# Optimization experiments

Hardware: AMD Instinct MI355X
Metric: run time of the kernel (lower is better)

## Reference

```python
import jax, jax.numpy as jnp
import numpy as np
from jax import lax

B, T, C = 4, 2048, 2048
H, S = 32, 64
HEAD_SIZE_DIVISOR = 8.0
LN_EPS = 1e-5


def setup_inputs() -> dict:
    key = jax.random.key(0)
    ks = jax.random.split(key, 12)
    scale = 0.02
    return {
        "hidden": jax.random.normal(ks[0], (B, T, C), jnp.float32),
        "state_kv": jnp.zeros((B, H, S, S), jnp.float32),
        "time_decay": jax.random.normal(ks[1], (H, S), jnp.float32) * 0.5,
        "time_faaaa": jax.random.normal(ks[2], (H, S), jnp.float32) * 0.5,
        "time_mix_key": jax.random.uniform(ks[3], (1, 1, C), jnp.float32),
        "time_mix_value": jax.random.uniform(ks[4], (1, 1, C), jnp.float32),
        "time_mix_receptance": jax.random.uniform(ks[5], (1, 1, C), jnp.float32),
        "time_mix_gate": jax.random.uniform(ks[6], (1, 1, C), jnp.float32),
        "key_w": jax.random.normal(ks[7], (C, C), jnp.float32) * scale,
        "value_w": jax.random.normal(ks[8], (C, C), jnp.float32) * scale,
        "receptance_w": jax.random.normal(ks[9], (C, C), jnp.float32) * scale,
        "gate_w": jax.random.normal(ks[10], (C, C), jnp.float32) * scale,
        "output_w": jax.random.normal(ks[11], (C, C), jnp.float32) * scale,
        "ln_w": jnp.ones((C,), jnp.float32),
        "ln_b": jnp.zeros((C,), jnp.float32),
    }


def _rwkv5_scan(r, k, v, w, u, state0):
    # r,k,v: [B,T,H,S]; w,u: [H,S]; state0: [B,H,S,S]
    w_ = w[None, :, :, None]  # decay broadcast over value dim
    u_ = u[None, :, :, None]  # time_first (bonus) broadcast over value dim

    def step(state, rkv):
        rt, kt, vt = rkv  # each [B,H,S]
        a = kt[:, :, :, None] * vt[:, :, None, :]      # outer product [B,H,S,S]
        o = jnp.einsum("bhs,bhsd->bhd", rt, u_ * a + state)
        state = a + w_ * state
        return state, o

    rt = jnp.moveaxis(r, 1, 0)  # [T,B,H,S]
    kt = jnp.moveaxis(k, 1, 0)
    vt = jnp.moveaxis(v, 1, 0)
    state_f, out = lax.scan(step, state0, (rt, kt, vt))
    return jnp.moveaxis(out, 0, 1), state_f  # [B,T,H,S], [B,H,S,S]


def reference(hidden, state_kv, time_decay, time_faaaa, time_mix_key,
              time_mix_value, time_mix_receptance, time_mix_gate,
              key_w, value_w, receptance_w, gate_w, output_w, ln_w, ln_b):
    B_, T_, C_ = hidden.shape
    H_, S_ = time_faaaa.shape

    # time shift: prepend zero row, drop last (state=None path)
    shifted = jnp.pad(hidden, ((0, 0), (1, 0), (0, 0)))[:, :-1]

    mix = lambda m: hidden * m + shifted * (1.0 - m)
    k = mix(time_mix_key) @ key_w.T
    v = mix(time_mix_value) @ value_w.T
    r = mix(time_mix_receptance) @ receptance_w.T
    gate = jax.nn.silu(mix(time_mix_gate) @ gate_w.T)

    r = r.reshape(B_, T_, H_, S_)
    k = k.reshape(B_, T_, H_, S_)
    v = v.reshape(B_, T_, H_, S_)

    w = jnp.exp(-jnp.exp(time_decay))  # [H,S]
    out, state_f = _rwkv5_scan(r, k, v, w, time_faaaa, state_kv)

    # GroupNorm over H groups of size S, applied per (b,t) row
    x = out.reshape(B_ * T_, H_, S_) / HEAD_SIZE_DIVISOR
    mu = jnp.mean(x, axis=-1, keepdims=True)
    var = jnp.var(x, axis=-1, keepdims=True)
    xn = (x - mu) * lax.rsqrt(var + LN_EPS)
    xn = xn.reshape(B_ * T_, H_ * S_) * ln_w + ln_b

    out = xn.reshape(B_, T_, C_) * gate
    out = out @ output_w.T
    return out, state_f
```

## Files before the change

kernel.cpp:

```cpp
#include <hip/hip_runtime.h>
#include <hip/hip_bf16.h>

typedef unsigned short u16;
typedef __bf16 bf16x8 __attribute__((ext_vector_type(8)));
typedef unsigned short ushort8v __attribute__((ext_vector_type(8)));
typedef float f32x4 __attribute__((ext_vector_type(4)));
typedef float f32x8 __attribute__((ext_vector_type(8)));

#define B_ 4
#define T_ 2048
#define C_ 2048
#define H_ 32
#define S_ 64

__device__ __forceinline__ u16 f2bf(float x) {
  unsigned int u = __float_as_uint(x);
  unsigned int r = (u + 0x7fffu + ((u >> 16) & 1u)) >> 16;
  return (u16)r;
}
__device__ __forceinline__ float bf2f(u16 x) {
  return __uint_as_float(((unsigned int)x) << 16);
}
__device__ __forceinline__ void gload_lds16(const void* g, void* l) {
  __builtin_amdgcn_global_load_lds(
      (const __attribute__((address_space(1))) void*)g,
      (__attribute__((address_space(3))) void*)l, 16, 0, 0);
}

#define VM10 asm volatile("s_waitcnt vmcnt(10)" ::: "memory")
#define VM8 asm volatile("s_waitcnt vmcnt(8)" ::: "memory")
#define VM4 asm volatile("s_waitcnt vmcnt(4)" ::: "memory")
#define VM0 asm volatile("s_waitcnt vmcnt(0)" ::: "memory")
#define BARR __builtin_amdgcn_s_barrier()
#define SCB __builtin_amdgcn_sched_barrier(0)

__global__ __launch_bounds__(256) void mix_cast_kernel(
    const float* __restrict__ hidden, const float* __restrict__ mixp,
    u16* __restrict__ out) {
  int idx = blockIdx.x * 256 + threadIdx.x;
  int c4 = idx & 511;
  int bt = idx >> 9;
  int t = bt & (T_ - 1);
  float4 h = reinterpret_cast<const float4*>(hidden)[idx];
  float4 m = reinterpret_cast<const float4*>(mixp)[c4];
  float4 sh = make_float4(0.f, 0.f, 0.f, 0.f);
  if (t != 0) sh = reinterpret_cast<const float4*>(hidden)[idx - 512];
  ushort4 o;
  o.x = f2bf(h.x * m.x + sh.x * (1.f - m.x));
  o.y = f2bf(h.y * m.y + sh.y * (1.f - m.y));
  o.z = f2bf(h.z * m.z + sh.z * (1.f - m.z));
  o.w = f2bf(h.w * m.w + sh.w * (1.f - m.w));
  reinterpret_cast<ushort4*>(out)[idx] = o;
}

__global__ __launch_bounds__(256) void mix4_cast_kernel(
    const float* __restrict__ hidden,
    const float* __restrict__ mK, const float* __restrict__ mV,
    const float* __restrict__ mR, const float* __restrict__ mG,
    u16* __restrict__ oK, u16* __restrict__ oV,
    u16* __restrict__ oR, u16* __restrict__ oG) {
  int idx = blockIdx.x * 256 + threadIdx.x;
  int c4 = idx & 511;
  int bt = idx >> 9;
  int t = bt & (T_ - 1);
  float4 h = reinterpret_cast<const float4*>(hidden)[idx];
  float4 sh = make_float4(0.f, 0.f, 0.f, 0.f);
  if (t != 0) sh = reinterpret_cast<const float4*>(hidden)[idx - 512];
  float4 m;
  ushort4 o;
#define DOMIX(MP, OP)                                          \
  m = reinterpret_cast<const float4*>(MP)[c4];                 \
  o.x = f2bf(h.x * m.x + sh.x * (1.f - m.x));                  \
  o.y = f2bf(h.y * m.y + sh.y * (1.f - m.y));                  \
  o.z = f2bf(h.z * m.z + sh.z * (1.f - m.z));                  \
  o.w = f2bf(h.w * m.w + sh.w * (1.f - m.w));                  \
  reinterpret_cast<ushort4*>(OP)[idx] = o;
  DOMIX(mK, oK)
  DOMIX(mV, oV)
  DOMIX(mR, oR)
  DOMIX(mG, oG)
#undef DOMIX
}

__global__ __launch_bounds__(256) void conv_bf16_kernel(
    const float* __restrict__ in, u16* __restrict__ out, int n4) {
  int i = blockIdx.x * 256 + threadIdx.x;
  if (i >= n4) return;
  float4 v = reinterpret_cast<const float4*>(in)[i];
  ushort4 o;
  o.x = f2bf(v.x); o.y = f2bf(v.y); o.z = f2bf(v.z); o.w = f2bf(v.w);
  reinterpret_cast<ushort4*>(out)[i] = o;
}

template <typename OT>
__global__ __launch_bounds__(512, 2) void gemm_bt256(
    const u16* __restrict__ A, const u16* __restrict__ Bm,
    OT* __restrict__ C, int M, int N, int K) {
  __shared__ u16 Asl[4][8192];
  __shared__ u16 Bsl[4][8192];
  const int tid = threadIdx.x, lane = tid & 63, w = tid >> 6;
  const int wr = w >> 2, wc = w & 3;
  const int nbn = N >> 8;
  const int nwg = gridDim.x, bid = blockIdx.x, cpx = nwg >> 3;
  const int swz = (bid & 7) * cpx + (bid >> 3);
  const int bm = swz / nbn, bn = swz % nbn;
  const int Ar0 = bm * 256, Br0 = bn * 256;

  const int rowoff = w * 32 + (lane >> 2);
  const int colswz = ((lane & 3) ^ ((lane >> 3) & 3)) * 8;
  const u16* Agl = A + (size_t)(Ar0 + rowoff) * K + colswz;
  const u16* Bgl = Bm + (size_t)(Br0 + rowoff) * K + colswz;
  const int lb = w * 1024;

  const int rdc = (((lane >> 4) ^ ((lane >> 1) & 3))) * 8;
  const int arow = wr * 128 + (lane & 15);
  const int brow = wc * 64 + (lane & 15);

  f32x4 acc[8][4];
#pragma unroll
  for (int m = 0; m < 8; m++)
#pragma unroll
    for (int n = 0; n < 4; n++) acc[m][n] = (f32x4){0.f, 0.f, 0.f, 0.f};

  auto STA = [&](int ktile, int kk, int slot) {
    const u16* g = Agl + ktile * 64 + kk * 32;
    gload_lds16(g, &Asl[slot][lb]);
    gload_lds16(g + (size_t)16 * K, &Asl[slot][lb + 512]);
  };
  auto STB = [&](int ktile, int kk, int slot) {
    const u16* g = Bgl + ktile * 64 + kk * 32;
    gload_lds16(g, &Bsl[slot][lb]);
    gload_lds16(g + (size_t)16 * K, &Bsl[slot][lb + 512]);
  };
  auto PH = [&](int P, int kk, int mh) {
    const u16* As_ = Asl[P * 2 + kk];
    const u16* Bs_ = Bsl[P * 2 + kk];
    bf16x8 af[4], bv[4];
    int ab = (arow + mh * 64) * 32 + rdc;
#pragma unroll
    for (int mf = 0; mf < 4; mf++)
      af[mf] = __builtin_bit_cast(bf16x8, *reinterpret_cast<const ushort8v*>(&As_[ab + mf * 512]));
    int bb = brow * 32 + rdc;
#pragma unroll
    for (int nf = 0; nf < 4; nf++)
      bv[nf] = __builtin_bit_cast(bf16x8, *reinterpret_cast<const ushort8v*>(&Bs_[bb + nf * 512]));
    __builtin_amdgcn_s_setprio(1);
#pragma unroll
    for (int mf = 0; mf < 4; mf++)
#pragma unroll
      for (int nf = 0; nf < 4; nf++)
        acc[mh * 4 + mf][nf] =
            __builtin_amdgcn_mfma_f32_16x16x32_bf16(af[mf], bv[nf], acc[mh * 4 + mf][nf], 0, 0, 0);
    __builtin_amdgcn_s_setprio(0);
  };

  const int NT = K >> 6;
  STA(0, 0, 0); STB(0, 0, 0);
  STA(0, 1, 1); STB(0, 1, 1);
  STA(1, 0, 2); STB(1, 0, 2);

  for (int T = 0; T + 2 < NT; ++T) {
    int P = T & 1, Q = P ^ 1;
    STA(T + 1, 1, Q * 2 + 1); VM10; BARR; SCB; PH(P, 0, 0); BARR;
    STB(T + 1, 1, Q * 2 + 1); VM10; BARR; SCB; PH(P, 0, 1); BARR;
    STA(T + 2, 0, P * 2 + 0); VM10; BARR; SCB; PH(P, 1, 0); BARR;
    STB(T + 2, 0, P * 2 + 0); VM10; BARR; SCB; PH(P, 1, 1); BARR;
  }
  {
    int T = NT - 2, P = T & 1, Q = P ^ 1;
    STA(T + 1, 1, Q * 2 + 1); VM10; BARR; SCB; PH(P, 0, 0); BARR;
    STB(T + 1, 1, Q * 2 + 1); VM10; BARR; SCB; PH(P, 0, 1); BARR;
    VM8; BARR; SCB; PH(P, 1, 0); BARR;
    VM8; BARR; SCB; PH(P, 1, 1); BARR;
  }
  {
    int P = (NT - 1) & 1;
    VM4; BARR; SCB; PH(P, 0, 0); BARR;
    VM4; BARR; SCB; PH(P, 0, 1); BARR;
    VM0; BARR; SCB; PH(P, 1, 0); BARR;
    VM0; BARR; SCB; PH(P, 1, 1);
  }

  int crow0 = Ar0 + wr * 128 + (lane >> 4) * 4;
  int ccol0 = Br0 + wc * 64 + (lane & 15);
#pragma unroll
  for (int mfg = 0; mfg < 8; mfg++) {
#pragma unroll
    for (int q = 0; q < 4; q++) {
      OT* cp = C + (size_t)(crow0 + mfg * 16 + q) * N + ccol0;
#pragma unroll
      for (int nf = 0; nf < 4; nf++) {
        if constexpr (sizeof(OT) == 2)
          cp[nf * 16] = (OT)f2bf(acc[mfg][nf][q]);
        else
          cp[nf * 16] = (OT)acc[mfg][nf][q];
      }
    }
  }
}

template <int CHL>
__global__ __launch_bounds__(128) void scan_phase1_mfma(
    const u16* __restrict__ Kb, const u16* __restrict__ Vb,
    const float* __restrict__ td, float* __restrict__ chunks) {
  constexpr int NCH = T_ / CHL;
  constexpr int LDW = CHL + 8;
  __shared__ u16 Ash[2][64 * LDW];
  __shared__ u16 Vsh[2][64 * LDW];
  int lane = threadIdx.x & 63, wib = threadIdx.x >> 6;
  int gw = blockIdx.x * 2 + wib;
  int c = gw & (NCH - 1), bh = gw / NCH;
  int h = bh & 31, b = bh >> 5;

  size_t base = ((size_t)b * T_ + (size_t)c * CHL) * C_ + h * 64 + lane;
  const u16* Kp = Kb + base;
  const u16* Vp = Vb + base;

  {
    float w = __expf(-__expf(td[h * 64 + lane]));
    u16* Arow = &Ash[wib][lane * LDW];
    float p = 1.f;
#pragma unroll
    for (int i4 = CHL - 4; i4 >= 0; i4 -= 4) {
      float a3 = bf2f(Kp[(size_t)(i4 + 3) * C_]) * p; p *= w;
      float a2 = bf2f(Kp[(size_t)(i4 + 2) * C_]) * p; p *= w;
      float a1 = bf2f(Kp[(size_t)(i4 + 1) * C_]) * p; p *= w;
      float a0 = bf2f(Kp[(size_t)(i4 + 0) * C_]) * p; p *= w;
      ushort4 pk;
      pk.x = f2bf(a0); pk.y = f2bf(a1); pk.z = f2bf(a2); pk.w = f2bf(a3);
      *reinterpret_cast<ushort4*>(&Arow[i4]) = pk;
    }
  }
  {
    u16* Vrow = &Vsh[wib][lane * LDW];
#pragma unroll
    for (int i4 = 0; i4 < CHL; i4 += 4) {
      ushort4 pk;
      pk.x = Vp[(size_t)(i4 + 0) * C_];
      pk.y = Vp[(size_t)(i4 + 1) * C_];
      pk.z = Vp[(size_t)(i4 + 2) * C_];
      pk.w = Vp[(size_t)(i4 + 3) * C_];
      *reinterpret_cast<ushort4*>(&Vrow[i4]) = pk;
    }
  }

  f32x4 acc[4][4];
#pragma unroll
  for (int m = 0; m < 4; m++)
#pragma unroll
    for (int n = 0; n < 4; n++) acc[m][n] = (f32x4){0.f, 0.f, 0.f, 0.f};

#pragma unroll
  for (int kb = 0; kb < CHL / 32; kb++) {
    int ko = kb * 32 + (lane >> 4) * 8;
    bf16x8 Af[4], Bf[4];
#pragma unroll
    for (int m = 0; m < 4; m++) {
      ushort8v t8 = *reinterpret_cast<const ushort8v*>(&Ash[wib][(m * 16 + (lane & 15)) * LDW + ko]);
      Af[m] = __builtin_bit_cast(bf16x8, t8);
    }
#pragma unroll
    for (int n = 0; n < 4; n++) {
      ushort8v t8 = *reinterpret_cast<const ushort8v*>(&Vsh[wib][(n * 16 + (lane & 15)) * LDW + ko]);
      Bf[n] = __builtin_bit_cast(bf16x8, t8);
    }
#pragma unroll
    for (int m = 0; m < 4; m++)
#pragma unroll
      for (int n = 0; n < 4; n++)
        acc[m][n] = __builtin_amdgcn_mfma_f32_16x16x32_bf16(Af[m], Bf[n], acc[m][n], 0, 0, 0);
  }

  float* outp = chunks + (((size_t)c * B_ + b) * H_ + h) * 4096;
  int r0 = (lane >> 4) * 4, c0 = lane & 15;
#pragma unroll
  for (int m = 0; m < 4; m++)
#pragma unroll
    for (int n = 0; n < 4; n++)
#pragma unroll
      for (int q = 0; q < 4; q++)
        outp[(size_t)(m * 16 + r0 + q) * 64 + n * 16 + c0] = acc[m][n][q];
}

template <int NCH, int CHL>
__global__ __launch_bounds__(256) void scan_phase1(
    const u16* __restrict__ Kb, const u16* __restrict__ Vb,
    const float* __restrict__ td, float* __restrict__ chunks) {
  int lane = threadIdx.x & 63;
  int gw = (blockIdx.x * 256 + threadIdx.x) >> 6;
  int c = gw & (NCH - 1), bh = gw / NCH;
  int h = bh & 31, b = bh >> 5;
  const float* tdh = td + h * 64;
  float wreg[64];
#pragma unroll
  for (int s = 0; s < 64; s++) wreg[s] = __expf(-__expf(tdh[s]));
  float st[64];
#pragma unroll
  for (int s = 0; s < 64; s++) st[s] = 0.f;
  size_t base = ((size_t)b * T_ + (size_t)c * CHL) * C_ + h * 64 + lane;
  const u16* Kp = Kb + base;
  const u16* Vp = Vb + base;
  for (int t = 0; t < CHL; t++) {
    float kcur = bf2f(Kp[(size_t)t * C_]), vcur = bf2f(Vp[(size_t)t * C_]);
#pragma unroll
    for (int s = 0; s < 64; s++) {
      float ks = __shfl(kcur, s);
      st[s] = fmaf(wreg[s], st[s], ks * vcur);
    }
  }
  float* outp = chunks + (((size_t)c * B_ + b) * H_ + h) * 4096 + lane;
#pragma unroll
  for (int s = 0; s < 64; s++) outp[s * 64] = st[s];
}

template <int NCH, int CHL>
__global__ __launch_bounds__(256) void scan_phase2(
    const float* __restrict__ st0, const float* __restrict__ td,
    float* __restrict__ chunks, float* __restrict__ state_out) {
  int idx = blockIdx.x * 256 + threadIdx.x;
  int h = (idx >> 12) & 31;
  int s = (idx >> 6) & 63;
  float wL = __expf(-(float)CHL * __expf(td[h * 64 + s]));
  float st = st0[idx];
#pragma unroll
  for (int cc = 0; cc < NCH; cc++) {
    size_t off = (size_t)cc * 524288 + idx;
    float sc = chunks[off];
    chunks[off] = st;
    st = fmaf(wL, st, sc);
  }
  state_out[idx] = st;
}

__global__ __launch_bounds__(256) void scan_phase3_mfma(
    const u16* __restrict__ Rb, const u16* __restrict__ Kb,
    const u16* __restrict__ Vb, const float* __restrict__ td,
    const float* __restrict__ tf, const float* __restrict__ chunks,
    const u16* __restrict__ Gb, const float* __restrict__ lnw,
    const float* __restrict__ lnb, u16* __restrict__ Y) {
  __shared__ __align__(16) u16 smem[4][5248];
  int lane = threadIdx.x & 63, wib = threadIdx.x >> 6;
  int gw = blockIdx.x * 4 + wib;
  int c = gw & 31, bh = gw >> 5;
  int h = bh & 31, b = bh >> 5;
  int a = lane & 15, g = lane >> 4;
  int h0 = h * 64;

  u16* Kt = smem[wib];
  u16* Vt = Kt + 1024;
  u16* StT = Vt + 1024;
  u16* AT = StT + 2560;

  f32x8 sA[2], sB[2], sC[2];
#pragma unroll
  for (int kk = 0; kk < 2; kk++) {
#pragma unroll
    for (int e = 0; e < 8; e++) {
      int s = kk * 32 + g * 8 + e;
      float ew = __expf(td[h0 + s]);
      sA[kk][e] = __expf(-(float)a * ew);
      sB[kk][e] = __expf(-((float)a - 8.f) * ew);
      sC[kk][e] = __expf(-(7.f - (float)a) * ew);
    }
  }
  f32x4 sE[4];
  f32x4 ewD;
#pragma unroll
  for (int ms = 0; ms < 4; ms++) {
    ewD[ms] = __expf(td[h0 + ms * 16 + a]);
#pragma unroll
    for (int q = 0; q < 4; q++)
      sE[ms][q] = __expf(-16.f * __expf(td[h0 + ms * 16 + g * 4 + q]));
  }

  f32x4 St[4][4];
  const float* cpc = chunks + (((size_t)c * B_ + b) * H_ + h) * 4096;
#pragma unroll
  for (int ms = 0; ms < 4; ms++)
#pragma unroll
    for (int nd = 0; nd < 4; nd++)
#pragma unroll
      for (int q = 0; q < 4; q++)
        St[ms][nd][q] = cpc[(size_t)(ms * 16 + g * 4 + q) * 64 + nd * 16 + a];

#pragma unroll
  for (int z = 0; z < 6; z++) {
    int idx = z * 64 + lane;
    int row = idx / 24, col = 16 + idx % 24;
    AT[row * 40 + col] = 0;
  }

  size_t tbase = ((size_t)b * T_ + (size_t)c * 64) * C_ + h0;

  for (int sb = 0; sb < 4; sb++) {
    size_t rb0 = tbase + (size_t)(sb * 16) * C_;

    ushort8v r8[2], k8[2];
#pragma unroll
    for (int kk = 0; kk < 2; kk++) {
      r8[kk] = *reinterpret_cast<const ushort8v*>(Rb + rb0 + (size_t)a * C_ + kk * 32 + g * 8);
      k8[kk] = *reinterpret_cast<const ushort8v*>(Kb + rb0 + (size_t)a * C_ + kk * 32 + g * 8);
    }
    {
      int srow = lane >> 3;
      int scol = (lane & 7) * 8;
      *reinterpret_cast<ushort8v*>(&Kt[srow * 64 + scol]) =
          *reinterpret_cast<const ushort8v*>(Kb + rb0 + (size_t)srow * C_ + scol);
      *reinterpret_cast<ushort8v*>(&Kt[(srow + 8) * 64 + scol]) =
          *reinterpret_cast<const ushort8v*>(Kb + rb0 + (size_t)(srow + 8) * C_ + scol);
      *reinterpret_cast<ushort8v*>(&Vt[srow * 64 + scol]) =
          *reinterpret_cast<const ushort8v*>(Vb + rb0 + (size_t)srow * C_ + scol);
      *reinterpret_cast<ushort8v*>(&Vt[(srow + 8) * 64 + scol]) =
          *reinterpret_cast<const ushort8v*>(Vb + rb0 + (size_t)(srow + 8) * C_ + scol);
    }

    f32x4 O[4];
#pragma unroll
    for (int nd = 0; nd < 4; nd++) O[nd] = (f32x4){0.f, 0.f, 0.f, 0.f};

#pragma unroll
    for (int kk = 0; kk < 2; kk++) {
#pragma unroll
      for (int msl = 0; msl < 2; msl++) {
        int ms = kk * 2 + msl;
#pragma unroll
        for (int nd = 0; nd < 4; nd++) {
          ushort4 pk;
          pk.x = f2bf(St[ms][nd][0]); pk.y = f2bf(St[ms][nd][1]);
          pk.z = f2bf(St[ms][nd][2]); pk.w = f2bf(St[ms][nd][3]);
          *reinterpret_cast<ushort4*>(&StT[(a + nd * 16) * 40 + msl * 16 + g * 4]) = pk;
        }
      }
      ushort8v rt;
#pragma unroll
      for (int e = 0; e < 8; e++) rt[e] = f2bf(bf2f(r8[kk][e]) * sA[kk][e]);
      bf16x8 rtf = __builtin_bit_cast(bf16x8, rt);
#pragma unroll
      for (int nd = 0; nd < 4; nd++) {
        ushort8v sfr = *reinterpret_cast<const ushort8v*>(&StT[(a + nd * 16) * 40 + g * 8]);
        O[nd] = __builtin_amdgcn_mfma_f32_16x16x32_bf16(
            rtf, __builtin_bit_cast(bf16x8, sfr), O[nd], 0, 0, 0);
      }
    }

    float p = 0.f;
    {
      uintptr_t ta = (uintptr_t)(tf + h0);
      asm volatile("" : "+v"(ta));
      const float* tfp = (const float*)ta;
#pragma unroll
      for (int kk = 0; kk < 2; kk++) {
        float4 t0 = *reinterpret_cast<const float4*>(tfp + kk * 32 + g * 8);
        float4 t1 = *reinterpret_cast<const float4*>(tfp + kk * 32 + g * 8 + 4);
        float tv[8] = {t0.x, t0.y, t0.z, t0.w, t1.x, t1.y, t1.z, t1.w};
#pragma unroll
        for (int e = 0; e < 8; e++)
          p = fmaf(bf2f(r8[kk][e]) * tv[e], bf2f(k8[kk][e]), p);
      }
    }
    p += __shfl_xor(p, 16);
    p += __shfl_xor(p, 32);

    f32x4 Am = (f32x4){0.f, 0.f, 0.f, 0.f};
#pragma unroll
    for (int kk = 0; kk < 2; kk++) {
      ushort8v kh, rh;
#pragma unroll
      for (int e = 0; e < 8; e++) {
        kh[e] = f2bf(bf2f(k8[kk][e]) * sC[kk][e]);
        rh[e] = f2bf(bf2f(r8[kk][e]) * sB[kk][e]);
      }
      Am = __builtin_amdgcn_mfma_f32_16x16x32_bf16(
          __builtin_bit_cast(bf16x8, kh), __builtin_bit_cast(bf16x8, rh), Am, 0, 0, 0);
    }
    {
      ushort4 aw;
#pragma unroll
      for (int q = 0; q < 4; q++) {
        int jr = g * 4 + q;
        float v = (jr < a) ? Am[q] : ((jr == a) ? p : 0.f);
        ((u16*)&aw)[q] = f2bf(v);
      }
      *reinterpret_cast<ushort4*>(&AT[a * 40 + g * 4]) = aw;
    }
    bf16x8 afrag;
    {
      ushort8v t8 = *reinterpret_cast<const ushort8v*>(&AT[a * 40 + g * 8]);
      afrag = __builtin_bit_cast(bf16x8, t8);
    }

    bf16x8 vfrag[4];
#pragma unroll
    for (int nd = 0; nd < 4; nd++) {
      ushort8v t8;
      if (g < 2) {
#pragma unroll
        for (int e = 0; e < 8; e++) t8[e] = Vt[(g * 8 + e) * 64 + a + nd * 16];
      } else {
#pragma unroll
        for (int e = 0; e < 8; e++) t8[e] = 0;
      }
      vfrag[nd] = __builtin_bit_cast(bf16x8, t8);
    }

#pragma unroll
    for (int nd = 0; nd < 4; nd++)
      O[nd] = __builtin_amdgcn_mfma_f32_16x16x32_bf16(afrag, vfrag[nd], O[nd], 0, 0, 0);

#pragma unroll
    for (int ms = 0; ms < 4; ms++)
#pragma unroll
      for (int nd = 0; nd < 4; nd++)
#pragma unroll
        for (int q = 0; q < 4; q++) St[ms][nd][q] *= sE[ms][q];

#pragma unroll
    for (int ms = 0; ms < 4; ms++) {
      ushort8v kt8;
      if (g < 2) {
#pragma unroll
        for (int e = 0; e < 8; e++) {
          int j = g * 8 + e;
          float f = bf2f(Kt[j * 64 + ms * 16 + a]) * __expf(-(15.f - (float)j) * ewD[ms]);
          kt8[e] = f2bf(f);
        }
      } else {
#pragma unroll
        for (int e = 0; e < 8; e++) kt8[e] = 0;
      }
      bf16x8 kf = __builtin_bit_cast(bf16x8, kt8);
#pragma unroll
      for (int nd = 0; nd < 4; nd++)
        St[ms][nd] = __builtin_amdgcn_mfma_f32_16x16x32_bf16(kf, vfrag[nd], St[ms][nd], 0, 0, 0);
    }

#pragma unroll
    for (int nd = 0; nd < 4; nd++)
#pragma unroll
      for (int q = 0; q < 4; q++) O[nd][q] *= 0.125f;
    {
      uintptr_t la = (uintptr_t)(lnw + h0);
      uintptr_t lba = (uintptr_t)(lnb + h0);
      asm volatile("" : "+v"(la), "+v"(lba));
      const float* lwp = (const float*)la;
      const float* lbp = (const float*)lba;
#pragma unroll
      for (int q = 0; q < 4; q++) {
        float ssum = O[0][q] + O[1][q] + O[2][q] + O[3][q];
        ssum += __shfl_xor(ssum, 1); ssum += __shfl_xor(ssum, 2);
        ssum += __shfl_xor(ssum, 4); ssum += __shfl_xor(ssum, 8);
        float mean = ssum * (1.f / 64.f);
        float vv = 0.f;
#pragma unroll
        for (int nd = 0; nd < 4; nd++) {
          float d = O[nd][q] - mean;
          vv = fmaf(d, d, vv);
        }
        vv += __shfl_xor(vv, 1); vv += __shfl_xor(vv, 2);
        vv += __shfl_xor(vv, 4); vv += __shfl_xor(vv, 8);
        float rs = rsqrtf(vv * (1.f / 64.f) + 1e-5f);
        size_t rowoff = rb0 + (size_t)(g * 4 + q) * C_;
#pragma unroll
        for (int nd = 0; nd < 4; nd++) {
          float xn = (O[nd][q] - mean) * rs;
          float gv = bf2f(Gb[rowoff + nd * 16 + a]);
          float sg = gv / (1.f + __expf(-gv));
          Y[rowoff + nd * 16 + a] = f2bf((xn * lwp[nd * 16 + a] + lbp[nd * 16 + a]) * sg);
        }
      }
    }
  }
}

template <int NCH, int CHL>
__global__ __launch_bounds__(256) void scan_phase3(
    const u16* __restrict__ Rb, const u16* __restrict__ Kb,
    const u16* __restrict__ Vb, const float* __restrict__ td,
    const float* __restrict__ tf, const float* __restrict__ chunks,
    const u16* __restrict__ Gb, const float* __restrict__ lnw,
    const float* __restrict__ lnb, u16* __restrict__ Y) {
  int lane = threadIdx.x & 63;
  int gw = (blockIdx.x * 256 + threadIdx.x) >> 6;
  int c = gw & (NCH - 1), bh = gw / NCH;
  int h = bh & 31, b = bh >> 5;
  const float* tdh = td + h * 64;
  float wreg[64];
#pragma unroll
  for (int s = 0; s < 64; s++) wreg[s] = __expf(-__expf(tdh[s]));
  float u_own = tf[h * 64 + lane];
  float lw = lnw[h * 64 + lane];
  float lb = lnb[h * 64 + lane];
  float st[64];
  const float* cp = chunks + (((size_t)c * B_ + b) * H_ + h) * 4096 + lane;
#pragma unroll
  for (int s = 0; s < 64; s++) st[s] = cp[s * 64];
  size_t base = ((size_t)b * T_ + (size_t)c * CHL) * C_ + h * 64 + lane;
  const u16* Rp = Rb + base;
  const u16* Kp = Kb + base;
  const u16* Vp = Vb + base;
  const u16* Gp = Gb + base;
  u16* Yp = Y + base;
  for (int t = 0; t < CHL; t++) {
    float rcur = bf2f(Rp[(size_t)t * C_]);
    float kcur = bf2f(Kp[(size_t)t * C_]);
    float vcur = bf2f(Vp[(size_t)t * C_]);
    float p = rcur * u_own * kcur;
#pragma unroll
    for (int off = 32; off >= 1; off >>= 1) p += __shfl_xor(p, off);
    float acc = 0.f;
#pragma unroll
    for (int s = 0; s < 64; s++) {
      float rs = __shfl(rcur, s);
      float ks = __shfl(kcur, s);
      acc = fmaf(rs, st[s], acc);
      st[s] = fmaf(wreg[s], st[s], ks * vcur);
    }
    float o = fmaf(p, vcur, acc);
    float x = o * 0.125f;
    float sum = x;
#pragma unroll
    for (int off = 32; off >= 1; off >>= 1) sum += __shfl_xor(sum, off);
    float mean = sum * (1.f / 64.f);
    float d = x - mean;
    float v2 = d * d;
#pragma unroll
    for (int off = 32; off >= 1; off >>= 1) v2 += __shfl_xor(v2, off);
    float var = v2 * (1.f / 64.f);
    float xn = d * rsqrtf(var + 1e-5f);
    float gg = bf2f(Gp[(size_t)t * C_]);
    float sg = gg / (1.f + __expf(-gg));
    Yp[(size_t)t * C_] = f2bf((xn * lw + lb) * sg);
  }
}

extern "C" void kernel_launch(void* const* d_in, const int* in_sizes, int n_in,
                              void* d_out, int out_size, void* d_ws, size_t ws_size,
                              hipStream_t stream) {
  const float* hidden = (const float*)d_in[0];
  const float* state0 = (const float*)d_in[1];
  const float* td = (const float*)d_in[2];
  const float* tf = (const float*)d_in[3];
  const float* mk = (const float*)d_in[4];
  const float* mv = (const float*)d_in[5];
  const float* mr = (const float*)d_in[6];
  const float* mg = (const float*)d_in[7];
  const float* kw = (const float*)d_in[8];
  const float* vw = (const float*)d_in[9];
  const float* rw = (const float*)d_in[10];
  const float* gw = (const float*)d_in[11];
  const float* ow = (const float*)d_in[12];
  const float* lnw = (const float*)d_in[13];
  const float* lnb = (const float*)d_in[14];

  float* out = (float*)d_out;
  float* state_f = out + (size_t)B_ * T_ * C_;

  const size_t MBe = (size_t)B_ * T_ * C_;
  const size_t chunks32 = (size_t)32 * B_ * H_ * S_ * S_ * 4;

  size_t bigNeed = 4 * MBe * 2 + (size_t)C_ * C_ * 2 + 4 * MBe * 2 + chunks32;
  bool useBig = (ws_size >= bigNeed);

  dim3 blk(256);
  int mixGrid = (B_ * T_ * C_ / 4) / 256;
  int convN4 = C_ * C_ / 4;
  int convGrid = convN4 / 256;
  int gemmGrid = (B_ * T_ / 256) * (C_ / 256);
  dim3 gblk(512);

  if (useBig) {
    char* ws = (char*)d_ws;
    u16* mixR = (u16*)ws;  ws += MBe * 2;
    u16* mixK = (u16*)ws;  ws += MBe * 2;
    u16* mixV = (u16*)ws;  ws += MBe * 2;
    u16* mixG = (u16*)ws;  ws += MBe * 2;
    u16* wb = (u16*)ws;    ws += (size_t)C_ * C_ * 2;
    u16* rb = (u16*)ws;    ws += MBe * 2;
    u16* kb = (u16*)ws;    ws += MBe * 2;
    u16* vb = (u16*)ws;    ws += MBe * 2;
    u16* gb = (u16*)ws;    ws += MBe * 2;
    float* chunks = (float*)ws;

    mix4_cast_kernel<<<mixGrid, blk, 0, stream>>>(hidden, mk, mv, mr, mg,
                                                  mixK, mixV, mixR, mixG);
    conv_bf16_kernel<<<convGrid, blk, 0, stream>>>(rw, wb, convN4);
    gemm_bt256<u16><<<gemmGrid, gblk, 0, stream>>>(mixR, wb, rb, B_ * T_, C_, C_);
    conv_bf16_kernel<<<convGrid, blk, 0, stream>>>(kw, wb, convN4);
    gemm_bt256<u16><<<gemmGrid, gblk, 0, stream>>>(mixK, wb, kb, B_ * T_, C_, C_);
    conv_bf16_kernel<<<convGrid, blk, 0, stream>>>(vw, wb, convN4);
    gemm_bt256<u16><<<gemmGrid, gblk, 0, stream>>>(mixV, wb, vb, B_ * T_, C_, C_);
    conv_bf16_kernel<<<convGrid, blk, 0, stream>>>(gw, wb, convN4);
    gemm_bt256<u16><<<gemmGrid, gblk, 0, stream>>>(mixG, wb, gb, B_ * T_, C_, C_);

    scan_phase1_mfma<64><<<(B_ * H_ * 32) / 2, dim3(128), 0, stream>>>(kb, vb, td, chunks);
    scan_phase2<32, 64><<<2048, blk, 0, stream>>>(state0, td, chunks, state_f);
    scan_phase3_mfma<<<(B_ * H_ * 32) / 4, blk, 0, stream>>>(rb, kb, vb, td, tf, chunks, gb, lnw, lnb, mixR);

    conv_bf16_kernel<<<convGrid, blk, 0, stream>>>(ow, wb, convN4);
    gemm_bt256<float><<<gemmGrid, gblk, 0, stream>>>(mixR, wb, out, B_ * T_, C_, C_);
    return;
  }

  char* ws = (char*)d_ws;
  u16* mixA = (u16*)ws;    ws += MBe * 2;
  u16* wb = (u16*)ws;      ws += (size_t)C_ * C_ * 2;
  u16* rb = (u16*)ws;      ws += MBe * 2;
  u16* kb = (u16*)ws;      ws += MBe * 2;
  u16* vb = (u16*)ws;      ws += MBe * 2;
  u16* gb = (u16*)ws;      ws += MBe * 2;
  float* chunks = (float*)ws;
  size_t fixed = (size_t)(ws - (char*)d_ws);
  bool use32 = (ws_size >= fixed + chunks32);

  mix_cast_kernel<<<mixGrid, blk, 0, stream>>>(hidden, mr, mixA);
  conv_bf16_kernel<<<convGrid, blk, 0, stream>>>(rw, wb, convN4);
  gemm_bt256<u16><<<gemmGrid, gblk, 0, stream>>>(mixA, wb, rb, B_ * T_, C_, C_);
  mix_cast_kernel<<<mixGrid, blk, 0, stream>>>(hidden, mk, mixA);
  conv_bf16_kernel<<<convGrid, blk, 0, stream>>>(kw, wb, convN4);
  gemm_bt256<u16><<<gemmGrid, gblk, 0, stream>>>(mixA, wb, kb, B_ * T_, C_, C_);
  mix_cast_kernel<<<mixGrid, blk, 0, stream>>>(hidden, mv, mixA);
  conv_bf16_kernel<<<convGrid, blk, 0, stream>>>(vw, wb, convN4);
  gemm_bt256<u16><<<gemmGrid, gblk, 0, stream>>>(mixA, wb, vb, B_ * T_, C_, C_);
  mix_cast_kernel<<<mixGrid, blk, 0, stream>>>(hidden, mg, mixA);
  conv_bf16_kernel<<<convGrid, blk, 0, stream>>>(gw, wb, convN4);
  gemm_bt256<u16><<<gemmGrid, gblk, 0, stream>>>(mixA, wb, gb, B_ * T_, C_, C_);

  if (use32) {
    scan_phase1_mfma<64><<<(B_ * H_ * 32) / 2, dim3(128), 0, stream>>>(kb, vb, td, chunks);
    scan_phase2<32, 64><<<2048, blk, 0, stream>>>(state0, td, chunks, state_f);
    scan_phase3_mfma<<<(B_ * H_ * 32) / 4, blk, 0, stream>>>(rb, kb, vb, td, tf, chunks, gb, lnw, lnb, mixA);
  } else {
    scan_phase1<16, 128><<<(B_ * H_ * 16) / 4, blk, 0, stream>>>(kb, vb, td, chunks);
    scan_phase2<16, 128><<<2048, blk, 0, stream>>>(state0, td, chunks, state_f);
    scan_phase3<16, 128><<<(B_ * H_ * 16) / 4, blk, 0, stream>>>(rb, kb, vb, td, tf, chunks, gb, lnw, lnb, mixA);
  }

  conv_bf16_kernel<<<convGrid, blk, 0, stream>>>(ow, wb, convN4);
  gemm_bt256<float><<<gemmGrid, gblk, 0, stream>>>(mixA, wb, out, B_ * T_, C_, C_);
}
```

Measured before the change: 734.2 us.

## Merge GEMM pipeline phases to halve barriers; launch scan kernels one wave per block

In the bf16 GEMM main loop, the A and B half-tile loads are issued together and two compute phases run between each pair of barriers, halving the number of block-wide barriers per K tile. The scan phase1 and phase3 kernels now run a single wavefront per block instead of packing two or four independent waves per block, which gives the scheduler finer-grained blocks and smaller LDS footprints. The cost is less interleaving of loads with compute inside the GEMM, plus larger issue bursts and more in-flight loads per wait.

```diff
diff --git a/kernel.cpp b/kernel.cpp
--- a/kernel.cpp
+++ b/kernel.cpp
@@ -161,24 +161,21 @@
 
   for (int T = 0; T + 2 < NT; ++T) {
     int P = T & 1, Q = P ^ 1;
-    STA(T + 1, 1, Q * 2 + 1); VM10; BARR; SCB; PH(P, 0, 0); BARR;
-    STB(T + 1, 1, Q * 2 + 1); VM10; BARR; SCB; PH(P, 0, 1); BARR;
-    STA(T + 2, 0, P * 2 + 0); VM10; BARR; SCB; PH(P, 1, 0); BARR;
-    STB(T + 2, 0, P * 2 + 0); VM10; BARR; SCB; PH(P, 1, 1); BARR;
+    STA(T + 1, 1, Q * 2 + 1); STB(T + 1, 1, Q * 2 + 1);
+    VM10; BARR; SCB; PH(P, 0, 0); PH(P, 0, 1); BARR;
+    STA(T + 2, 0, P * 2 + 0); STB(T + 2, 0, P * 2 + 0);
+    VM10; BARR; SCB; PH(P, 1, 0); PH(P, 1, 1); BARR;
   }
   {
     int T = NT - 2, P = T & 1, Q = P ^ 1;
-    STA(T + 1, 1, Q * 2 + 1); VM10; BARR; SCB; PH(P, 0, 0); BARR;
-    STB(T + 1, 1, Q * 2 + 1); VM10; BARR; SCB; PH(P, 0, 1); BARR;
-    VM8; BARR; SCB; PH(P, 1, 0); BARR;
-    VM8; BARR; SCB; PH(P, 1, 1); BARR;
+    STA(T + 1, 1, Q * 2 + 1); STB(T + 1, 1, Q * 2 + 1);
+    VM10; BARR; SCB; PH(P, 0, 0); PH(P, 0, 1); BARR;
+    VM8; BARR; SCB; PH(P, 1, 0); PH(P, 1, 1); BARR;
   }
   {
     int P = (NT - 1) & 1;
-    VM4; BARR; SCB; PH(P, 0, 0); BARR;
-    VM4; BARR; SCB; PH(P, 0, 1); BARR;
-    VM0; BARR; SCB; PH(P, 1, 0); BARR;
-    VM0; BARR; SCB; PH(P, 1, 1);
+    VM4; BARR; SCB; PH(P, 0, 0); PH(P, 0, 1); BARR;
+    VM0; BARR; SCB; PH(P, 1, 0); PH(P, 1, 1);
   }
 
   int crow0 = Ar0 + wr * 128 + (lane >> 4) * 4;
@@ -200,15 +197,15 @@
 }
 
 template <int CHL>
-__global__ __launch_bounds__(128) void scan_phase1_mfma(
+__global__ __launch_bounds__(64) void scan_phase1_mfma(
     const u16* __restrict__ Kb, const u16* __restrict__ Vb,
     const float* __restrict__ td, float* __restrict__ chunks) {
   constexpr int NCH = T_ / CHL;
   constexpr int LDW = CHL + 8;
-  __shared__ u16 Ash[2][64 * LDW];
-  __shared__ u16 Vsh[2][64 * LDW];
-  int lane = threadIdx.x & 63, wib = threadIdx.x >> 6;
-  int gw = blockIdx.x * 2 + wib;
+  __shared__ u16 Ash[64 * LDW];
+  __shared__ u16 Vsh[64 * LDW];
+  int lane = threadIdx.x & 63;
+  int gw = blockIdx.x;
   int c = gw & (NCH - 1), bh = gw / NCH;
   int h = bh & 31, b = bh >> 5;
 
@@ -218,7 +215,7 @@
 
   {
     float w = __expf(-__expf(td[h * 64 + lane]));
-    u16* Arow = &Ash[wib][lane * LDW];
+    u16* Arow = &Ash[lane * LDW];
     float p = 1.f;
 #pragma unroll
     for (int i4 = CHL - 4; i4 >= 0; i4 -= 4) {
@@ -232,7 +229,7 @@
     }
   }
   {
-    u16* Vrow = &Vsh[wib][lane * LDW];
+    u16* Vrow = &Vsh[lane * LDW];
 #pragma unroll
     for (int i4 = 0; i4 < CHL; i4 += 4) {
       ushort4 pk;
@@ -256,12 +253,12 @@
     bf16x8 Af[4], Bf[4];
 #pragma unroll
     for (int m = 0; m < 4; m++) {
-      ushort8v t8 = *reinterpret_cast<const ushort8v*>(&Ash[wib][(m * 16 + (lane & 15)) * LDW + ko]);
+      ushort8v t8 = *reinterpret_cast<const ushort8v*>(&Ash[(m * 16 + (lane & 15)) * LDW + ko]);
       Af[m] = __builtin_bit_cast(bf16x8, t8);
     }
 #pragma unroll
     for (int n = 0; n < 4; n++) {
-      ushort8v t8 = *reinterpret_cast<const ushort8v*>(&Vsh[wib][(n * 16 + (lane & 15)) * LDW + ko]);
+      ushort8v t8 = *reinterpret_cast<const ushort8v*>(&Vsh[(n * 16 + (lane & 15)) * LDW + ko]);
       Bf[n] = __builtin_bit_cast(bf16x8, t8);
     }
 #pragma unroll
@@ -332,21 +329,21 @@
   state_out[idx] = st;
 }
 
-__global__ __launch_bounds__(256) void scan_phase3_mfma(
+__global__ __launch_bounds__(64) void scan_phase3_mfma(
     const u16* __restrict__ Rb, const u16* __restrict__ Kb,
     const u16* __restrict__ Vb, const float* __restrict__ td,
     const float* __restrict__ tf, const float* __restrict__ chunks,
     const u16* __restrict__ Gb, const float* __restrict__ lnw,
     const float* __restrict__ lnb, u16* __restrict__ Y) {
-  __shared__ __align__(16) u16 smem[4][5248];
-  int lane = threadIdx.x & 63, wib = threadIdx.x >> 6;
-  int gw = blockIdx.x * 4 + wib;
+  __shared__ __align__(16) u16 smem[5248];
+  int lane = threadIdx.x & 63;
+  int gw = blockIdx.x;
   int c = gw & 31, bh = gw >> 5;
   int h = bh & 31, b = bh >> 5;
   int a = lane & 15, g = lane >> 4;
   int h0 = h * 64;
 
-  u16* Kt = smem[wib];
+  u16* Kt = smem;
   u16* Vt = Kt + 1024;
   u16* StT = Vt + 1024;
   u16* AT = StT + 2560;
@@ -692,9 +689,9 @@
     conv_bf16_kernel<<<convGrid, blk, 0, stream>>>(gw, wb, convN4);
     gemm_bt256<u16><<<gemmGrid, gblk, 0, stream>>>(mixG, wb, gb, B_ * T_, C_, C_);
 
-    scan_phase1_mfma<64><<<(B_ * H_ * 32) / 2, dim3(128), 0, stream>>>(kb, vb, td, chunks);
+    scan_phase1_mfma<64><<<B_ * H_ * 32, dim3(64), 0, stream>>>(kb, vb, td, chunks);
     scan_phase2<32, 64><<<2048, blk, 0, stream>>>(state0, td, chunks, state_f);
-    scan_phase3_mfma<<<(B_ * H_ * 32) / 4, blk, 0, stream>>>(rb, kb, vb, td, tf, chunks, gb, lnw, lnb, mixR);
+    scan_phase3_mfma<<<B_ * H_ * 32, dim3(64), 0, stream>>>(rb, kb, vb, td, tf, chunks, gb, lnw, lnb, mixR);
 
     conv_bf16_kernel<<<convGrid, blk, 0, stream>>>(ow, wb, convN4);
     gemm_bt256<float><<<gemmGrid, gblk, 0, stream>>>(mixR, wb, out, B_ * T_, C_, C_);
@@ -726,9 +723,9 @@
   gemm_bt256<u16><<<gemmGrid, gblk, 0, stream>>>(mixA, wb, gb, B_ * T_, C_, C_);
 
   if (use32) {
-    scan_phase1_mfma<64><<<(B_ * H_ * 32) / 2, dim3(128), 0, stream>>>(kb, vb, td, chunks);
+    scan_phase1_mfma<64><<<B_ * H_ * 32, dim3(64), 0, stream>>>(kb, vb, td, chunks);
     scan_phase2<32, 64><<<2048, blk, 0, stream>>>(state0, td, chunks, state_f);
-    scan_phase3_mfma<<<(B_ * H_ * 32) / 4, blk, 0, stream>>>(rb, kb, vb, td, tf, chunks, gb, lnw, lnb, mixA);
+    scan_phase3_mfma<<<B_ * H_ * 32, dim3(64), 0, stream>>>(rb, kb, vb, td, tf, chunks, gb, lnw, lnb, mixA);
   } else {
     scan_phase1<16, 128><<<(B_ * H_ * 16) / 4, blk, 0, stream>>>(kb, vb, td, chunks);
     scan_phase2<16, 128><<<2048, blk, 0, stream>>>(state0, td, chunks, state_f);
```

New measurement: 716.1 us. -2.5%, faster.
